# Kernel optimization log

Measured on AMD Instinct MI355X. Metric: run time of the kernel, lower is better.

## Reference

```python
import jax, jax.numpy as jnp
import numpy as np

D = 1024   # feature_dim
K = 10     # num_anchors
B = 16384  # batch
H = 8      # num_heads


def setup_inputs() -> dict:
    key = jax.random.key(0)
    ks = jax.random.split(key, 12)
    f32 = jnp.float32

    def w(k, shape, scale=0.02):
        return (jax.random.normal(k, shape, f32) * scale)

    return {
        "features": jax.random.normal(ks[0], (B, D), f32),
        "anchors": w(ks[1], (K, D), 0.1),
        # anchor_refiner: Linear(D, D//2) -> ReLU -> Linear(D//2, D) -> Tanh
        "ar_w1": w(ks[2], (D, D // 2)), "ar_b1": jnp.zeros((D // 2,), f32),
        "ar_w2": w(ks[3], (D // 2, D)), "ar_b2": jnp.zeros((D,), f32),
        # attention projections
        "q_w": w(ks[4], (D, D)), "q_b": jnp.zeros((D,), f32),
        "k_w": w(ks[5], (D, D)), "k_b": jnp.zeros((D,), f32),
        "v_w": w(ks[6], (D, D)), "v_b": jnp.zeros((D,), f32),
        "o_w": w(ks[7], (D, D)), "o_b": jnp.zeros((D,), f32),
        # feature_enhancer: LayerNorm -> Linear(D,2D) -> GELU -> Linear(2D,D)
        "ln_g": jnp.ones((D,), f32), "ln_b": jnp.zeros((D,), f32),
        "ff_w1": w(ks[8], (D, 2 * D)), "ff_b1": jnp.zeros((2 * D,), f32),
        "ff_w2": w(ks[9], (2 * D, D)), "ff_b2": jnp.zeros((D,), f32),
        "div_w": jnp.asarray(0.001, f32),
        "cen_w": jnp.asarray(0.001, f32),
    }


def _l2norm(x, eps=1e-8):
    n = jnp.linalg.norm(x, axis=-1, keepdims=True)
    return x / jnp.maximum(n, eps)


def _layernorm(x, g, b, eps=1e-5):
    mu = jnp.mean(x, axis=-1, keepdims=True)
    var = jnp.mean(jnp.square(x - mu), axis=-1, keepdims=True)
    return (x - mu) * jax.lax.rsqrt(var + eps) * g + b


def reference(features, anchors, ar_w1, ar_b1, ar_w2, ar_b2,
              q_w, q_b, k_w, k_b, v_w, v_b, o_w, o_b,
              ln_g, ln_b, ff_w1, ff_b1, ff_w2, ff_b2, div_w, cen_w):
    b = features.shape[0]
    hd = D // H
    fn = _l2norm(features)                                 # [B, D]

    # anchor refinement
    refin = jnp.tanh(jax.nn.relu(anchors @ ar_w1 + ar_b1) @ ar_w2 + ar_b2)
    an = _l2norm(anchors + 0.1 * refin)                    # [K, D]

    # multi-head cross-attention to anchors
    q = (fn @ q_w + q_b).reshape(b, H, hd)                 # [B, H, hd]
    k = (an @ k_w + k_b).reshape(K, H, hd)                 # [K, H, hd]
    v = (an @ v_w + v_b).reshape(K, H, hd)
    scores = jnp.einsum('bhd,khd->bhk', q, k) / jnp.sqrt(jnp.asarray(hd, fn.dtype))
    aw = jax.nn.softmax(scores, axis=-1)                   # [B, H, K]
    att = jnp.einsum('bhk,khd->bhd', aw, v).reshape(b, D)
    att = att @ o_w + o_b

    # feature enhancer (dropout inactive: eval mode)
    enh = fn + 0.1 * att
    h = jax.nn.gelu(_layernorm(enh, ln_g, ln_b) @ ff_w1 + ff_b1, approximate=False)
    enh = h @ ff_w2 + ff_b2
    final = fn + 0.2 * enh                                 # [B, D]

    # diversity loss: pdist over K=10 anchors (45 pairs)
    diff = an[:, None, :] - an[None, :, :]                 # [K, K, D]
    dmat = jnp.sqrt(jnp.maximum(jnp.sum(diff * diff, -1), 1e-24))
    iu = np.triu_indices(K, 1)
    div_loss = jnp.exp(-jnp.maximum(dmat[iu].mean(), 1e-6))

    # center loss: attention-weighted feature-anchor distances
    avg_att = aw.mean(axis=1)                              # [B, K]
    sq = (jnp.sum(fn * fn, 1, keepdims=True) + jnp.sum(an * an, 1)
          - 2.0 * fn @ an.T)
    fa_dist = jnp.sqrt(jnp.maximum(sq, 1e-12))             # [B, K]
    center_loss = jnp.sum(avg_att * fa_dist, axis=1).mean()

    geo = jnp.abs(div_w) * div_loss + jnp.abs(cen_w) * center_loss
    geo = jnp.clip(geo, 0.0, 0.01)
    return final, geo
```

## Files before the change

### kernel.cpp

```cpp
#include <hip/hip_runtime.h>
#include <hip/hip_bf16.h>
#include <math.h>

typedef __hip_bfloat16 bf16;

#define D_  1024
#define K_  10
#define B_  16384
#define H_  8
#define HD_ 128

struct alignas(16) BF8 { bf16 v[8]; };
struct alignas(8)  BF4 { bf16 v[4]; };

typedef __bf16 bf8v __attribute__((ext_vector_type(8)));
typedef float  f4v  __attribute__((ext_vector_type(4)));

__device__ __forceinline__ float b2f(bf16 x){ return __bfloat162float(x); }
__device__ __forceinline__ bf16  f2b(float x){ return __float2bfloat16(x); }

#define GL2LDS16(g, l) __builtin_amdgcn_global_load_lds( \
    (__attribute__((address_space(1))) void*)(g), \
    (__attribute__((address_space(3))) void*)(l), 16, 0, 0)

__global__ __launch_bounds__(256) void l2norm_k(const float* __restrict__ x,
                                                bf16* __restrict__ fnb) {
  int b = blockIdx.x, t = threadIdx.x;
  float4 v = ((const float4*)(x + (size_t)b * D_))[t];
  float p = v.x*v.x + v.y*v.y + v.z*v.z + v.w*v.w;
  #pragma unroll
  for (int o = 32; o > 0; o >>= 1) p += __shfl_down(p, o);
  __shared__ float wsum[4];
  if ((t & 63) == 0) wsum[t >> 6] = p;
  __syncthreads();
  __shared__ float inv_s;
  if (t == 0) inv_s = 1.f / fmaxf(sqrtf(wsum[0]+wsum[1]+wsum[2]+wsum[3]), 1e-8f);
  __syncthreads();
  float iv = inv_s;
  BF4 o;
  o.v[0] = f2b(v.x*iv); o.v[1] = f2b(v.y*iv);
  o.v[2] = f2b(v.z*iv); o.v[3] = f2b(v.w*iv);
  ((BF4*)(fnb + (size_t)b * D_))[t] = o;
}

__global__ __launch_bounds__(256) void wt_k(const float* __restrict__ w,
                                            bf16* __restrict__ wt, int R, int C) {
  __shared__ float tle[32][33];
  int c0 = blockIdx.x * 32, r0 = blockIdx.y * 32;
  int tx = threadIdx.x & 31, ty = threadIdx.x >> 5;
  #pragma unroll
  for (int i = 0; i < 32; i += 8)
    tle[ty + i][tx] = w[(size_t)(r0 + ty + i) * C + c0 + tx];
  __syncthreads();
  #pragma unroll
  for (int i = 0; i < 32; i += 8)
    wt[(size_t)(c0 + ty + i) * R + r0 + tx] = f2b(tle[tx][ty + i]);
}

template<int COLS, int KD, int ACT>
__global__ __launch_bounds__(256) void panelmm_k(
    const float* __restrict__ A, const float* __restrict__ W,
    const float* __restrict__ bias, const float* __restrict__ aux,
    float* __restrict__ out,
    const float* __restrict__ W2, const float* __restrict__ bias2,
    float* __restrict__ out2, int N, int npanel) {
  constexpr int GROUPS = 256 / COLS;
  constexpr int DCH = KD / GROUPS;
  __shared__ float A_s[K_][KD];
  __shared__ float part[K_][COLS][GROUPS];
  const int t = threadIdx.x;
  int blk = blockIdx.x;
  const float* Wm = W; const float* bm = bias; float* om = out;
  if (blk >= npanel) { blk -= npanel; Wm = W2; bm = bias2; om = out2; }
  const int panel = blk;
  for (int i = t; i < K_*KD; i += 256) A_s[0][i] = A[i];
  __syncthreads();
  const int cg = t % COLS, g = t / COLS;
  const int col = panel*COLS + cg;
  float s[K_];
  #pragma unroll
  for (int r = 0; r < K_; ++r) s[r] = 0.f;
  const float* wp = Wm + (size_t)(g*DCH)*N + col;
  for (int d = g*DCH; d < (g+1)*DCH; ++d) {
    float wv = *wp; wp += N;
    #pragma unroll
    for (int r = 0; r < K_; ++r) s[r] = fmaf(A_s[r][d], wv, s[r]);
  }
  #pragma unroll
  for (int r = 0; r < K_; ++r) part[r][cg][g] = s[r];
  __syncthreads();
  for (int o = t; o < K_*COLS; o += 256) {
    int r = o / COLS, c = o % COLS;
    float v = 0.f;
    #pragma unroll
    for (int gg = 0; gg < GROUPS; ++gg) v += part[r][c][gg];
    v += bm[panel*COLS + c];
    if constexpr (ACT == 1) v = fmaxf(v, 0.f);
    if constexpr (ACT == 2) v = aux[(size_t)r*N + panel*COLS + c] + 0.1f*tanhf(v);
    om[(size_t)r*N + panel*COLS + c] = v;
  }
}

template<int TRANSOUT, typename TW>
__global__ __launch_bounds__(256) void smallmm_k(
    const float* __restrict__ A, const TW* __restrict__ W,
    bf16* __restrict__ outb, float scale) {
  constexpr int COLS = 64, GROUPS = 4, DCH = 32, NW = 1024;
  __shared__ float A_s[K_][128];
  __shared__ float part[K_][COLS][GROUPS];
  const int t = threadIdx.x;
  const int h = blockIdx.x & 7, panel = blockIdx.x >> 3;
  for (int i = t; i < K_*128; i += 256) {
    int r = i >> 7, j = i & 127;
    A_s[r][j] = A[r*1024 + h*128 + j];
  }
  __syncthreads();
  const int cg = t % COLS, g = t / COLS;
  const int col = panel*COLS + cg;
  float s[K_];
  #pragma unroll
  for (int r = 0; r < K_; ++r) s[r] = 0.f;
  const TW* wp = W + (size_t)(h*128 + g*DCH)*NW + col;
  for (int d = g*DCH; d < g*DCH + DCH; ++d) {
    float wv;
    if constexpr (sizeof(TW) == 2) wv = b2f(*wp); else wv = *wp;
    wp += NW;
    #pragma unroll
    for (int r = 0; r < K_; ++r) s[r] = fmaf(A_s[r][d], wv, s[r]);
  }
  #pragma unroll
  for (int r = 0; r < K_; ++r) part[r][cg][g] = s[r];
  __syncthreads();
  for (int o = t; o < 16*COLS; o += 256) {
    int r = o / COLS, c = o % COLS;
    float v = 0.f;
    if (r < K_) {
      #pragma unroll
      for (int gg = 0; gg < GROUPS; ++gg) v += part[r][c][gg];
      v *= scale;
    }
    if constexpr (TRANSOUT) outb[(size_t)(panel*COLS + c)*128 + h*16 + r] = f2b(v);
    else                    outb[(size_t)(h*16 + r)*NW + panel*COLS + c] = f2b(v);
  }
}

__global__ void sbias_k(const float* __restrict__ qb, const float* __restrict__ Km,
                        float* __restrict__ sb) {
  int c = threadIdx.x;
  int h = c >> 4, k = c & 15;
  float s = 0.f;
  if (k < K_) {
    for (int j = 0; j < HD_; ++j)
      s = fmaf(qb[h*HD_ + j], Km[(size_t)k*D_ + h*HD_ + j], s);
  }
  sb[c] = s * 0.08838834764831845f;
}

__global__ __launch_bounds__(256) void ar3_k(const float* __restrict__ an_un,
    float* __restrict__ an, float* __restrict__ na, float* __restrict__ divloss) {
  __shared__ float a_s[K_][D_];
  __shared__ float nrm[K_];
  __shared__ float dm[45];
  const int t = threadIdx.x;
  for (int i = t; i < K_*D_; i += 256) a_s[0][i] = an_un[i];
  __syncthreads();
  const int wid = t >> 6, lane = t & 63;
  for (int r = wid; r < K_; r += 4) {
    float p = 0.f;
    for (int j = lane; j < D_; j += 64) p += a_s[r][j]*a_s[r][j];
    #pragma unroll
    for (int o = 1; o < 64; o <<= 1) p += __shfl_xor(p, o);
    if (lane == 0) nrm[r] = p;
  }
  __syncthreads();
  for (int i = t; i < K_*D_; i += 256) {
    int r = i >> 10;
    float iv = 1.f / fmaxf(sqrtf(nrm[r]), 1e-8f);
    float v = a_s[0][i] * iv;
    a_s[0][i] = v;
    an[i] = v;
  }
  if (t < K_) {
    float iv = 1.f / fmaxf(sqrtf(nrm[t]), 1e-8f);
    na[t] = nrm[t] * iv * iv;
  }
  __syncthreads();
  const int pr = t >> 2, sub = t & 3;
  if (pr < 45) {
    int i = 0, j = 0, c = pr;
    for (i = 0; i < K_; ++i) { int cnt = K_-1-i; if (c < cnt) { j = i+1+c; break; } c -= cnt; }
    float s = 0.f;
    for (int d = sub*256; d < sub*256 + 256; ++d) {
      float df = a_s[i][d] - a_s[j][d]; s += df*df;
    }
    s += __shfl_xor(s, 1); s += __shfl_xor(s, 2);
    if (sub == 0) dm[pr] = sqrtf(fmaxf(s, 1e-24f));
  }
  __syncthreads();
  if (t == 0) {
    float m = 0.f;
    for (int p = 0; p < 45; ++p) m += dm[p];
    m *= (1.f/45.f);
    *divloss = expf(-fmaxf(m, 1e-6f));
  }
}

template<int EPI, typename TO>
__global__ __launch_bounds__(256) void mgemm_k(
    const bf16* __restrict__ A, const bf16* __restrict__ Bt,
    const float* __restrict__ bias, const bf16* __restrict__ aux,
    TO* __restrict__ out, int M, int N, int Kd, float scale) {
  constexpr int BM = 128, BN = 128, BK = 32;
  __shared__ bf16 As[BM][BK];
  __shared__ bf16 Bs[BN][BK];
  const int tid = threadIdx.x;
  const int nMB = M / BM;
  const int nwg = gridDim.x;
  int wg = blockIdx.x;
  wg = (wg & 7) * (nwg >> 3) + (wg >> 3);
  const int mb = wg % nMB, nb = wg / nMB;
  const int bm = mb * BM, bn = nb * BN;

  const int srow = tid >> 2;
  const int sk   = (tid & 3) * 8;
  const bf16* ga = A  + (size_t)(bm + srow) * Kd + sk;
  const bf16* gb = Bt + (size_t)(bn + srow) * Kd + sk;
  const size_t rstep = (size_t)64 * Kd;
  bf16* la = &As[0][0] + tid * 8;
  bf16* lb = &Bs[0][0] + tid * 8;

  const int w    = tid >> 6;
  const int lane = tid & 63;
  const int wr = (w >> 1) * 64, wc = (w & 1) * 64;
  const int fr = lane & 15, fg = lane >> 4;

  f4v acc[4][4];
  const f4v zz = {0.f, 0.f, 0.f, 0.f};
  #pragma unroll
  for (int m = 0; m < 4; ++m)
    #pragma unroll
    for (int n = 0; n < 4; ++n) acc[m][n] = zz;

  for (int k0 = 0; k0 < Kd; k0 += BK) {
    GL2LDS16(ga,         la);
    GL2LDS16(ga + rstep, la + 2048);
    GL2LDS16(gb,         lb);
    GL2LDS16(gb + rstep, lb + 2048);
    __syncthreads();
    bf8v af[4], bf_[4];
    #pragma unroll
    for (int m = 0; m < 4; ++m)
      af[m] = *(const bf8v*)&As[wr + m*16 + fr][fg*8];
    #pragma unroll
    for (int n = 0; n < 4; ++n)
      bf_[n] = *(const bf8v*)&Bs[wc + n*16 + fr][fg*8];
    #pragma unroll
    for (int m = 0; m < 4; ++m)
      #pragma unroll
      for (int n = 0; n < 4; ++n)
        acc[m][n] = __builtin_amdgcn_mfma_f32_16x16x32_bf16(af[m], bf_[n], acc[m][n], 0, 0, 0);
    __syncthreads();
    ga += BK; gb += BK;
  }

  float bv[4];
  #pragma unroll
  for (int n = 0; n < 4; ++n) bv[n] = bias[bn + wc + n*16 + fr];
  #pragma unroll
  for (int m = 0; m < 4; ++m) {
    #pragma unroll
    for (int r = 0; r < 4; ++r) {
      const int row = bm + wr + m*16 + fg*4 + r;
      #pragma unroll
      for (int n = 0; n < 4; ++n) {
        const int col = bn + wc + n*16 + fr;
        float x = acc[m][n][r] + bv[n];
        if constexpr (EPI == 1) x = b2f(aux[(size_t)row * N + col]) + scale * x;
        if constexpr (EPI == 2) x = 0.5f * x * (1.f + erff(x * 0.70710678118654752f));
        if constexpr (sizeof(TO) == 2) out[(size_t)row * N + col] = f2b(x);
        else                           out[(size_t)row * N + col] = x;
      }
    }
  }
}

template<int EPI, typename TO>
__global__ __launch_bounds__(512, 2) void mgemm256_k(
    const bf16* __restrict__ A, const bf16* __restrict__ Bt,
    const float* __restrict__ bias, const bf16* __restrict__ aux,
    TO* __restrict__ out, int M, int N, int Kd, float scale) {
  constexpr int BM = 256, BN = 256, BK = 32, DEPTH = 3;
  __shared__ bf16 As[DEPTH][BM*BK];
  __shared__ bf16 Bs[DEPTH][BN*BK];
  const int tid = threadIdx.x;
  const int nMB = M / BM;
  const int nwg = gridDim.x;
  int wg = blockIdx.x;
  wg = (wg & 7) * (nwg >> 3) + (wg >> 3);
  const int bm = (wg % nMB) * BM, bn = (wg / nMB) * BN;

  const int sr = tid >> 2, ss = tid & 3;
  const int sx = ((ss ^ (sr & 3)) * 8);
  const bf16* gA0 = A  + (size_t)(bm + sr)       * Kd + sx;
  const bf16* gA1 = A  + (size_t)(bm + sr + 128) * Kd + sx;
  const bf16* gB0 = Bt + (size_t)(bn + sr)       * Kd + sx;
  const bf16* gB1 = Bt + (size_t)(bn + sr + 128) * Kd + sx;

  const int wid = tid >> 6, lane = tid & 63;
  const int wm = wid >> 2, wn = wid & 3;
  const int fr = lane & 15, fg = lane >> 4;
  const int slot = (fg ^ (fr & 3)) * 8;

  f4v acc[8][4];
  const f4v zz = {0.f, 0.f, 0.f, 0.f};
  #pragma unroll
  for (int m = 0; m < 8; ++m)
    #pragma unroll
    for (int n = 0; n < 4; ++n) acc[m][n] = zz;

  const int nt = Kd / BK;
  #pragma unroll
  for (int p = 0; p < DEPTH; ++p) {
    const int ko = p * BK;
    GL2LDS16(gA0 + ko, &As[p][0] + tid*8);
    GL2LDS16(gA1 + ko, &As[p][0] + tid*8 + 4096);
    GL2LDS16(gB0 + ko, &Bs[p][0] + tid*8);
    GL2LDS16(gB1 + ko, &Bs[p][0] + tid*8 + 4096);
  }

  int bufi = 0;
  for (int t = 0; t < nt; ++t) {
    const int rem = nt - 1 - t;
    if (rem >= 2)      asm volatile("s_waitcnt vmcnt(8)" ::: "memory");
    else if (rem == 1) asm volatile("s_waitcnt vmcnt(4)" ::: "memory");
    else               asm volatile("s_waitcnt vmcnt(0)" ::: "memory");
    __builtin_amdgcn_s_barrier();
    asm volatile("" ::: "memory");
    const bf16* la = &As[bufi][0];
    const bf16* lb = &Bs[bufi][0];
    bf8v af[8], bq[4];
    #pragma unroll
    for (int m = 0; m < 8; ++m)
      af[m] = *(const bf8v*)(la + (wm*128 + m*16 + fr)*BK + slot);
    #pragma unroll
    for (int n = 0; n < 4; ++n)
      bq[n] = *(const bf8v*)(lb + (wn*64 + n*16 + fr)*BK + slot);
    asm volatile("s_waitcnt lgkmcnt(0)" ::: "memory");
    __builtin_amdgcn_s_barrier();
    asm volatile("" ::: "memory");
    if (t + DEPTH < nt) {
      const int ko = (t + DEPTH) * BK;
      GL2LDS16(gA0 + ko, &As[bufi][0] + tid*8);
      GL2LDS16(gA1 + ko, &As[bufi][0] + tid*8 + 4096);
      GL2LDS16(gB0 + ko, &Bs[bufi][0] + tid*8);
      GL2LDS16(gB1 + ko, &Bs[bufi][0] + tid*8 + 4096);
    }
    __builtin_amdgcn_s_setprio(1);
    #pragma unroll
    for (int m = 0; m < 8; ++m)
      #pragma unroll
      for (int n = 0; n < 4; ++n)
        acc[m][n] = __builtin_amdgcn_mfma_f32_16x16x32_bf16(af[m], bq[n], acc[m][n], 0, 0, 0);
    __builtin_amdgcn_s_setprio(0);
    bufi = (bufi == DEPTH-1) ? 0 : bufi + 1;
  }

  float bv[4];
  #pragma unroll
  for (int n = 0; n < 4; ++n) bv[n] = bias[bn + wn*64 + n*16 + fr];
  #pragma unroll
  for (int m = 0; m < 8; ++m) {
    #pragma unroll
    for (int r = 0; r < 4; ++r) {
      const int row = bm + wm*128 + m*16 + fg*4 + r;
      #pragma unroll
      for (int n = 0; n < 4; ++n) {
        const int col = bn + wn*64 + n*16 + fr;
        float x = acc[m][n][r] + bv[n];
        if constexpr (EPI == 1) x = b2f(aux[(size_t)row * N + col]) + scale * x;
        if constexpr (EPI == 2) x = 0.5f * x * (1.f + erff(x * 0.70710678118654752f));
        if constexpr (sizeof(TO) == 2) out[(size_t)row * N + col] = f2b(x);
        else                           out[(size_t)row * N + col] = x;
      }
    }
  }
}

__device__ __forceinline__ BF8 pack8(float4 a, float4 b){
  BF8 o;
  o.v[0]=f2b(a.x); o.v[1]=f2b(a.y); o.v[2]=f2b(a.z); o.v[3]=f2b(a.w);
  o.v[4]=f2b(b.x); o.v[5]=f2b(b.y); o.v[6]=f2b(b.z); o.v[7]=f2b(b.w);
  return o;
}

__global__ __launch_bounds__(256) void attn2_k(
    const float* __restrict__ S, const bf16* __restrict__ fn,
    const float* __restrict__ an, const float* __restrict__ na,
    bf16* __restrict__ awp, float* __restrict__ cen_acc) {
  __shared__ bf16 Ab[K_][D_];
  __shared__ float na_s[K_];
  __shared__ float cred[4];
  const int t = threadIdx.x;
  for (int i = t*8; i < K_*D_; i += 2048) {
    float4 a0 = *(const float4*)(an+i), a1 = *(const float4*)(an+i+4);
    *(BF8*)(&Ab[0][0]+i) = pack8(a0, a1);
  }
  if (t < K_) na_s[t] = na[t];
  __syncthreads();
  const int wid = t >> 6, lane = t & 63;
  const int d0 = lane * 16;
  const int sub = lane & 7, head = lane >> 3;
  const int k0 = sub*2, k1 = k0 + 1;
  float na0 = (k0 < K_) ? na_s[k0] : 0.f;
  float na1 = (k1 < K_) ? na_s[k1] : 0.f;
  float c_acc = 0.f;
  const int row0 = blockIdx.x * 32 + wid * 8;

  for (int i = 0; i < 8; ++i) {
    const int row = row0 + i;
    float2 sv = *(const float2*)(S + (size_t)row*128 + head*16 + k0);
    float v0 = (k0 < K_) ? sv.x : -1e30f;
    float v1 = (k1 < K_) ? sv.y : -1e30f;
    float m = fmaxf(v0, v1);
    m = fmaxf(m, __shfl_xor(m,1)); m = fmaxf(m, __shfl_xor(m,2)); m = fmaxf(m, __shfl_xor(m,4));
    float e0 = (k0 < K_) ? __expf(v0 - m) : 0.f;
    float e1 = (k1 < K_) ? __expf(v1 - m) : 0.f;
    float es = e0 + e1;
    es += __shfl_xor(es,1); es += __shfl_xor(es,2); es += __shfl_xor(es,4);
    float inv = 1.f / es;
    float a0 = e0 * inv, a1 = e1 * inv;
    bf16 b0 = f2b(a0), b1 = f2b(a1);
    unsigned int pk = (unsigned int)(*(unsigned short*)&b0)
                    | ((unsigned int)(*(unsigned short*)&b1) << 16);
    *(unsigned int*)(awp + (size_t)row*128 + head*16 + k0) = pk;
    float g0 = a0, g1 = a1;
    g0 += __shfl_xor(g0,8); g0 += __shfl_xor(g0,16); g0 += __shfl_xor(g0,32);
    g1 += __shfl_xor(g1,8); g1 += __shfl_xor(g1,16); g1 += __shfl_xor(g1,32);
    const BF8* fr = (const BF8*)(fn + (size_t)row*D_) + lane*2;
    BF8 f0 = fr[0], f1 = fr[1];
    float fv[16];
    #pragma unroll
    for (int j = 0; j < 8; ++j) { fv[j] = b2f(f0.v[j]); fv[8+j] = b2f(f1.v[j]); }
    float my0 = 0.f, my1 = 0.f;
    #pragma unroll
    for (int k = 0; k < K_; ++k) {
      BF8 aa = *(const BF8*)&Ab[k][d0];
      BF8 ab = *(const BF8*)&Ab[k][d0 + 8];
      float s = 0.f;
      #pragma unroll
      for (int j = 0; j < 8; ++j) {
        s = fmaf(fv[j],   b2f(aa.v[j]), s);
        s = fmaf(fv[8+j], b2f(ab.v[j]), s);
      }
      #pragma unroll
      for (int o = 1; o < 64; o <<= 1) s += __shfl_xor(s, o);
      my0 = (k == k0) ? s : my0;
      my1 = (k == k1) ? s : my1;
    }
    if (sub < 5) {
      float dist0 = sqrtf(fmaxf(1.f + na0 - 2.f*my0, 1e-12f));
      float dist1 = sqrtf(fmaxf(1.f + na1 - 2.f*my1, 1e-12f));
      c_acc = fmaf(g0, dist0, c_acc);
      c_acc = fmaf(g1, dist1, c_acc);
    }
  }
  #pragma unroll
  for (int o = 1; o < 64; o <<= 1) c_acc += __shfl_xor(c_acc, o);
  if (lane == 0) cred[wid] = c_acc;
  __syncthreads();
  if (t == 0) {
    float s = (cred[0]+cred[1]+cred[2]+cred[3]) * (1.f/64.f/(float)B_);
    atomicAdd(cen_acc, s);
  }
}

__global__ __launch_bounds__(256) void ln_k(const bf16* __restrict__ x,
    const float* __restrict__ g, const float* __restrict__ bta,
    bf16* __restrict__ out) {
  int b = blockIdx.x, t = threadIdx.x;
  BF4 ld = ((const BF4*)(x + (size_t)b * D_))[t];
  float v[4];
  #pragma unroll
  for (int j = 0; j < 4; ++j) v[j] = b2f(ld.v[j]);
  float s = v[0]+v[1]+v[2]+v[3];
  #pragma unroll
  for (int o = 32; o > 0; o >>= 1) s += __shfl_down(s, o);
  __shared__ float w1[4], w2[4];
  if ((t & 63) == 0) w1[t >> 6] = s;
  __syncthreads();
  __shared__ float mu_s, rs_s;
  if (t == 0) mu_s = (w1[0]+w1[1]+w1[2]+w1[3]) * (1.f/D_);
  __syncthreads();
  float mu = mu_s;
  float qv = 0.f;
  #pragma unroll
  for (int j = 0; j < 4; ++j) { float d = v[j]-mu; qv += d*d; }
  #pragma unroll
  for (int o = 32; o > 0; o >>= 1) qv += __shfl_down(qv, o);
  if ((t & 63) == 0) w2[t >> 6] = qv;
  __syncthreads();
  if (t == 0) rs_s = rsqrtf((w2[0]+w2[1]+w2[2]+w2[3]) * (1.f/D_) + 1e-5f);
  __syncthreads();
  float rs = rs_s;
  BF4 o;
  #pragma unroll
  for (int j = 0; j < 4; ++j) {
    int col = t*4 + j;
    o.v[j] = f2b((v[j]-mu)*rs*g[col] + bta[col]);
  }
  ((BF4*)(out + (size_t)b * D_))[t] = o;
}

__global__ void geo_k(const float* __restrict__ divl, const float* __restrict__ cen,
                      const float* __restrict__ div_w, const float* __restrict__ cen_w,
                      float* __restrict__ out) {
  float g = fabsf(*div_w) * (*divl) + fabsf(*cen_w) * (*cen);
  out[0] = fminf(fmaxf(g, 0.f), 0.01f);
}

extern "C" void kernel_launch(void* const* d_in, const int* in_sizes, int n_in,
                              void* d_out, int out_size, void* d_ws, size_t ws_size,
                              hipStream_t stream) {
  const float* features = (const float*)d_in[0];
  const float* anchors  = (const float*)d_in[1];
  const float* ar_w1 = (const float*)d_in[2];
  const float* ar_b1 = (const float*)d_in[3];
  const float* ar_w2 = (const float*)d_in[4];
  const float* ar_b2 = (const float*)d_in[5];
  const float* q_w = (const float*)d_in[6];
  const float* q_b = (const float*)d_in[7];
  const float* k_w = (const float*)d_in[8];
  const float* k_b = (const float*)d_in[9];
  const float* v_w = (const float*)d_in[10];
  const float* v_b = (const float*)d_in[11];
  const float* o_w = (const float*)d_in[12];
  const float* o_b = (const float*)d_in[13];
  const float* ln_g = (const float*)d_in[14];
  const float* ln_b = (const float*)d_in[15];
  const float* ff_w1 = (const float*)d_in[16];
  const float* ff_b1 = (const float*)d_in[17];
  const float* ff_w2 = (const float*)d_in[18];
  const float* ff_b2 = (const float*)d_in[19];
  const float* div_w = (const float*)d_in[20];
  const float* cen_w = (const float*)d_in[21];
  float* out = (float*)d_out;

  char* w = (char*)d_ws;
  bf16* ws_fnb = (bf16*)w;  w += (size_t)B_ * D_ * 2;
  bf16* ws_enh = (bf16*)w;  w += (size_t)B_ * D_ * 2;
  bf16* ws_ln  = (bf16*)w;  w += (size_t)B_ * D_ * 2;
  bf16* ws_h   = (bf16*)w;  w += (size_t)B_ * 2048 * 2;
  float* ws_S  = (float*)w; w += (size_t)B_ * 128 * 4;
  bf16* ws_awp = (bf16*)w;  w += (size_t)B_ * 128 * 2;
  bf16* ws_wq  = (bf16*)w;  w += (size_t)D_ * D_ * 2;
  bf16* ws_w1t = (bf16*)w;  w += (size_t)D_ * 2048 * 2;
  bf16* ws_w2t = (bf16*)w;  w += (size_t)2048 * D_ * 2;
  bf16* ws_wt  = (bf16*)w;  w += (size_t)128 * D_ * 2;
  bf16* ws_vt  = (bf16*)w;  w += (size_t)D_ * 128 * 2;
  float* ws_har = (float*)w;  w += (size_t)K_ * (D_/2) * 4;
  float* ws_anu = (float*)w;  w += (size_t)K_ * D_ * 4;
  float* ws_an  = (float*)w;  w += (size_t)K_ * D_ * 4;
  float* ws_k   = (float*)w;  w += (size_t)K_ * D_ * 4;
  float* ws_v   = (float*)w;  w += (size_t)K_ * D_ * 4;
  float* ws_na  = (float*)w;  w += 256;
  float* ws_div = (float*)w;  w += 256;
  float* ws_cen = (float*)w;  w += 256;
  float* ws_sb  = (float*)w;  w += 512;
  if ((size_t)(w - (char*)d_ws) > ws_size) return;

  hipMemsetAsync(ws_cen, 0, 4, stream);

  wt_k<<<dim3(D_/32,   D_/32),   256, 0, stream>>>(q_w,   ws_wq,  D_,   D_);
  wt_k<<<dim3(2048/32, D_/32),   256, 0, stream>>>(ff_w1, ws_w1t, D_,   2048);
  wt_k<<<dim3(D_/32,   2048/32), 256, 0, stream>>>(ff_w2, ws_w2t, 2048, D_);

  l2norm_k<<<B_, 256, 0, stream>>>(features, ws_fnb);

  panelmm_k<32, 1024, 1><<<16, 256, 0, stream>>>(
      anchors, ar_w1, ar_b1, nullptr, ws_har,
      nullptr, nullptr, nullptr, D_/2, 16);
  panelmm_k<64, 512, 2><<<16, 256, 0, stream>>>(
      ws_har, ar_w2, ar_b2, anchors, ws_anu,
      nullptr, nullptr, nullptr, D_, 16);
  ar3_k<<<1, 256, 0, stream>>>(ws_anu, ws_an, ws_na, ws_div);
  panelmm_k<64, 1024, 0><<<32, 256, 0, stream>>>(
      ws_an, k_w, k_b, nullptr, ws_k,
      v_w, v_b, ws_v, D_, 16);

  smallmm_k<0, bf16><<<128, 256, 0, stream>>>(ws_k, ws_wq, ws_wt, 0.08838834764831845f);
  sbias_k<<<1, 128, 0, stream>>>(q_b, ws_k, ws_sb);
  smallmm_k<1, float><<<128, 256, 0, stream>>>(ws_v, o_w, ws_vt, 1.f);

  mgemm_k<0, float><<<dim3((B_/128)*(128/128)), 256, 0, stream>>>(
      ws_fnb, ws_wt, ws_sb, nullptr, ws_S, B_, 128, D_, 0.f);

  attn2_k<<<B_/32, 256, 0, stream>>>(ws_S, ws_fnb, ws_an, ws_na, ws_awp, ws_cen);

  mgemm256_k<1, bf16><<<dim3((B_/256)*(D_/256)), 512, 0, stream>>>(
      ws_awp, ws_vt, o_b, ws_fnb, ws_enh, B_, D_, 128, 0.1f);

  ln_k<<<B_, 256, 0, stream>>>(ws_enh, ln_g, ln_b, ws_ln);

  mgemm256_k<2, bf16><<<dim3((B_/256)*(2048/256)), 512, 0, stream>>>(
      ws_ln, ws_w1t, ff_b1, nullptr, ws_h, B_, 2048, D_, 0.f);

  mgemm256_k<1, float><<<dim3((B_/256)*(D_/256)), 512, 0, stream>>>(
      ws_h, ws_w2t, ff_b2, ws_fnb, out, B_, D_, 2048, 0.2f);

  geo_k<<<1, 1, 0, stream>>>(ws_div, ws_cen, div_w, cen_w, out + (size_t)B_ * D_);
}
```

Baseline: 446.1 us.

## Fold feature-anchor distances into score GEMM and deepen GEMM pipeline

Appends -2*anchor rows to the score weight matrix and 1+|a|^2 bias entries, so the score GEMM also produces squared feature-anchor distances, and the attention kernel stops re-reading the normalized features to compute dot products. The 256-tile GEMM also moves to a 4-stage LDS pipeline with prefetch issued right after the barrier, drops the second barrier per iteration, and splits the fragment loads to overlap with MFMAs. This doubles the score GEMM's N, raises LDS usage, and relies on a power-of-two DEPTH for the slot masking.

```diff
diff --git a/kernel.cpp b/kernel.cpp
--- a/kernel.cpp
+++ b/kernel.cpp
@@ -145,15 +145,36 @@
 }
 
 __global__ void sbias_k(const float* __restrict__ qb, const float* __restrict__ Km,
-                        float* __restrict__ sb) {
+                        const float* __restrict__ na, float* __restrict__ sb) {
   int c = threadIdx.x;
-  int h = c >> 4, k = c & 15;
-  float s = 0.f;
+  if (c < 128) {
+    int h = c >> 4, k = c & 15;
+    float s = 0.f;
+    if (k < K_) {
+      for (int j = 0; j < HD_; ++j)
+        s = fmaf(qb[h*HD_ + j], Km[(size_t)k*D_ + h*HD_ + j], s);
+    }
+    sb[c] = s * 0.08838834764831845f;
+  } else {
+    int j = c - 128;
+    sb[c] = (j < K_) ? (1.f + na[j]) : 0.f;
+  }
+}
+
+__global__ __launch_bounds__(256) void anext_k(const float* __restrict__ an,
+                                               bf16* __restrict__ wt) {
+  int k = blockIdx.x;
+  bf16* dst = wt + (size_t)(128 + k) * 1024;
+  int i = threadIdx.x * 4;
+  BF4 o;
   if (k < K_) {
-    for (int j = 0; j < HD_; ++j)
-      s = fmaf(qb[h*HD_ + j], Km[(size_t)k*D_ + h*HD_ + j], s);
-  }
-  sb[c] = s * 0.08838834764831845f;
+    float4 a = *(const float4*)(an + (size_t)k*1024 + i);
+    o.v[0] = f2b(-2.f*a.x); o.v[1] = f2b(-2.f*a.y);
+    o.v[2] = f2b(-2.f*a.z); o.v[3] = f2b(-2.f*a.w);
+  } else {
+    o.v[0] = o.v[1] = o.v[2] = o.v[3] = f2b(0.f);
+  }
+  *(BF4*)(dst + i) = o;
 }
 
 __global__ __launch_bounds__(256) void ar3_k(const float* __restrict__ an_un,
@@ -289,7 +310,7 @@
     const bf16* __restrict__ A, const bf16* __restrict__ Bt,
     const float* __restrict__ bias, const bf16* __restrict__ aux,
     TO* __restrict__ out, int M, int N, int Kd, float scale) {
-  constexpr int BM = 256, BN = 256, BK = 32, DEPTH = 3;
+  constexpr int BM = 256, BN = 256, BK = 32, DEPTH = 4;
   __shared__ bf16 As[DEPTH][BM*BK];
   __shared__ bf16 Bs[DEPTH][BN*BK];
   const int tid = threadIdx.x;
@@ -309,7 +330,7 @@
   const int wid = tid >> 6, lane = tid & 63;
   const int wm = wid >> 2, wn = wid & 3;
   const int fr = lane & 15, fg = lane >> 4;
-  const int slot = (fg ^ (fr & 3)) * 8;
+  const int rslot = (fg ^ (fr & 3)) * 8;
 
   f4v acc[8][4];
   const f4v zz = {0.f, 0.f, 0.f, 0.f};
@@ -320,49 +341,63 @@
 
   const int nt = Kd / BK;
   #pragma unroll
-  for (int p = 0; p < DEPTH; ++p) {
-    const int ko = p * BK;
-    GL2LDS16(gA0 + ko, &As[p][0] + tid*8);
-    GL2LDS16(gA1 + ko, &As[p][0] + tid*8 + 4096);
-    GL2LDS16(gB0 + ko, &Bs[p][0] + tid*8);
-    GL2LDS16(gB1 + ko, &Bs[p][0] + tid*8 + 4096);
-  }
-
-  int bufi = 0;
+  for (int p = 0; p < DEPTH-1; ++p) {
+    if (p < nt) {
+      const int ko = p * BK;
+      GL2LDS16(gA0 + ko, &As[p][0] + tid*8);
+      GL2LDS16(gA1 + ko, &As[p][0] + tid*8 + 4096);
+      GL2LDS16(gB0 + ko, &Bs[p][0] + tid*8);
+      GL2LDS16(gB1 + ko, &Bs[p][0] + tid*8 + 4096);
+    }
+  }
+
   for (int t = 0; t < nt; ++t) {
     const int rem = nt - 1 - t;
     if (rem >= 2)      asm volatile("s_waitcnt vmcnt(8)" ::: "memory");
     else if (rem == 1) asm volatile("s_waitcnt vmcnt(4)" ::: "memory");
     else               asm volatile("s_waitcnt vmcnt(0)" ::: "memory");
+    __builtin_amdgcn_sched_barrier(0);
     __builtin_amdgcn_s_barrier();
-    asm volatile("" ::: "memory");
-    const bf16* la = &As[bufi][0];
-    const bf16* lb = &Bs[bufi][0];
+    __builtin_amdgcn_sched_barrier(0);
+    if (t + DEPTH - 1 < nt) {
+      const int st = t + DEPTH - 1;
+      const int sl = st & (DEPTH-1);
+      const int ko = st * BK;
+      GL2LDS16(gA0 + ko, &As[sl][0] + tid*8);
+      GL2LDS16(gA1 + ko, &As[sl][0] + tid*8 + 4096);
+      GL2LDS16(gB0 + ko, &Bs[sl][0] + tid*8);
+      GL2LDS16(gB1 + ko, &Bs[sl][0] + tid*8 + 4096);
+    }
+    const int slot = t & (DEPTH-1);
+    const bf16* la = &As[slot][0];
+    const bf16* lb = &Bs[slot][0];
     bf8v af[8], bq[4];
     #pragma unroll
-    for (int m = 0; m < 8; ++m)
-      af[m] = *(const bf8v*)(la + (wm*128 + m*16 + fr)*BK + slot);
+    for (int m = 0; m < 4; ++m)
+      af[m] = *(const bf8v*)(la + (wm*128 + m*16 + fr)*BK + rslot);
     #pragma unroll
     for (int n = 0; n < 4; ++n)
-      bq[n] = *(const bf8v*)(lb + (wn*64 + n*16 + fr)*BK + slot);
+      bq[n] = *(const bf8v*)(lb + (wn*64 + n*16 + fr)*BK + rslot);
+    __builtin_amdgcn_sched_barrier(0);
+    #pragma unroll
+    for (int m = 4; m < 8; ++m)
+      af[m] = *(const bf8v*)(la + (wm*128 + m*16 + fr)*BK + rslot);
+    asm volatile("s_waitcnt lgkmcnt(4)" ::: "memory");
+    __builtin_amdgcn_sched_barrier(0);
+    __builtin_amdgcn_s_setprio(1);
+    #pragma unroll
+    for (int m = 0; m < 4; ++m)
+      #pragma unroll
+      for (int n = 0; n < 4; ++n)
+        acc[m][n] = __builtin_amdgcn_mfma_f32_16x16x32_bf16(af[m], bq[n], acc[m][n], 0, 0, 0);
     asm volatile("s_waitcnt lgkmcnt(0)" ::: "memory");
-    __builtin_amdgcn_s_barrier();
-    asm volatile("" ::: "memory");
-    if (t + DEPTH < nt) {
-      const int ko = (t + DEPTH) * BK;
-      GL2LDS16(gA0 + ko, &As[bufi][0] + tid*8);
-      GL2LDS16(gA1 + ko, &As[bufi][0] + tid*8 + 4096);
-      GL2LDS16(gB0 + ko, &Bs[bufi][0] + tid*8);
-      GL2LDS16(gB1 + ko, &Bs[bufi][0] + tid*8 + 4096);
-    }
-    __builtin_amdgcn_s_setprio(1);
-    #pragma unroll
-    for (int m = 0; m < 8; ++m)
+    __builtin_amdgcn_sched_barrier(0);
+    #pragma unroll
+    for (int m = 4; m < 8; ++m)
       #pragma unroll
       for (int n = 0; n < 4; ++n)
         acc[m][n] = __builtin_amdgcn_mfma_f32_16x16x32_bf16(af[m], bq[n], acc[m][n], 0, 0, 0);
     __builtin_amdgcn_s_setprio(0);
-    bufi = (bufi == DEPTH-1) ? 0 : bufi + 1;
   }
 
   float bv[4];
@@ -386,39 +421,21 @@
   }
 }
 
-__device__ __forceinline__ BF8 pack8(float4 a, float4 b){
-  BF8 o;
-  o.v[0]=f2b(a.x); o.v[1]=f2b(a.y); o.v[2]=f2b(a.z); o.v[3]=f2b(a.w);
-  o.v[4]=f2b(b.x); o.v[5]=f2b(b.y); o.v[6]=f2b(b.z); o.v[7]=f2b(b.w);
-  return o;
-}
-
 __global__ __launch_bounds__(256) void attn2_k(
-    const float* __restrict__ S, const bf16* __restrict__ fn,
-    const float* __restrict__ an, const float* __restrict__ na,
-    bf16* __restrict__ awp, float* __restrict__ cen_acc) {
-  __shared__ bf16 Ab[K_][D_];
-  __shared__ float na_s[K_];
+    const float* __restrict__ S, bf16* __restrict__ awp,
+    float* __restrict__ cen_acc) {
   __shared__ float cred[4];
   const int t = threadIdx.x;
-  for (int i = t*8; i < K_*D_; i += 2048) {
-    float4 a0 = *(const float4*)(an+i), a1 = *(const float4*)(an+i+4);
-    *(BF8*)(&Ab[0][0]+i) = pack8(a0, a1);
-  }
-  if (t < K_) na_s[t] = na[t];
-  __syncthreads();
   const int wid = t >> 6, lane = t & 63;
-  const int d0 = lane * 16;
   const int sub = lane & 7, head = lane >> 3;
   const int k0 = sub*2, k1 = k0 + 1;
-  float na0 = (k0 < K_) ? na_s[k0] : 0.f;
-  float na1 = (k1 < K_) ? na_s[k1] : 0.f;
   float c_acc = 0.f;
   const int row0 = blockIdx.x * 32 + wid * 8;
 
   for (int i = 0; i < 8; ++i) {
     const int row = row0 + i;
-    float2 sv = *(const float2*)(S + (size_t)row*128 + head*16 + k0);
+    const float* Sr = S + (size_t)row * 256;
+    float2 sv = *(const float2*)(Sr + head*16 + k0);
     float v0 = (k0 < K_) ? sv.x : -1e30f;
     float v1 = (k1 < K_) ? sv.y : -1e30f;
     float m = fmaxf(v0, v1);
@@ -436,32 +453,11 @@
     float g0 = a0, g1 = a1;
     g0 += __shfl_xor(g0,8); g0 += __shfl_xor(g0,16); g0 += __shfl_xor(g0,32);
     g1 += __shfl_xor(g1,8); g1 += __shfl_xor(g1,16); g1 += __shfl_xor(g1,32);
-    const BF8* fr = (const BF8*)(fn + (size_t)row*D_) + lane*2;
-    BF8 f0 = fr[0], f1 = fr[1];
-    float fv[16];
-    #pragma unroll
-    for (int j = 0; j < 8; ++j) { fv[j] = b2f(f0.v[j]); fv[8+j] = b2f(f1.v[j]); }
-    float my0 = 0.f, my1 = 0.f;
-    #pragma unroll
-    for (int k = 0; k < K_; ++k) {
-      BF8 aa = *(const BF8*)&Ab[k][d0];
-      BF8 ab = *(const BF8*)&Ab[k][d0 + 8];
-      float s = 0.f;
-      #pragma unroll
-      for (int j = 0; j < 8; ++j) {
-        s = fmaf(fv[j],   b2f(aa.v[j]), s);
-        s = fmaf(fv[8+j], b2f(ab.v[j]), s);
-      }
-      #pragma unroll
-      for (int o = 1; o < 64; o <<= 1) s += __shfl_xor(s, o);
-      my0 = (k == k0) ? s : my0;
-      my1 = (k == k1) ? s : my1;
-    }
     if (sub < 5) {
-      float dist0 = sqrtf(fmaxf(1.f + na0 - 2.f*my0, 1e-12f));
-      float dist1 = sqrtf(fmaxf(1.f + na1 - 2.f*my1, 1e-12f));
-      c_acc = fmaf(g0, dist0, c_acc);
-      c_acc = fmaf(g1, dist1, c_acc);
+      float d20 = Sr[128 + k0];
+      float d21 = Sr[128 + k1];
+      c_acc = fmaf(g0, sqrtf(fmaxf(d20, 1e-12f)), c_acc);
+      c_acc = fmaf(g1, sqrtf(fmaxf(d21, 1e-12f)), c_acc);
     }
   }
   #pragma unroll
@@ -550,12 +546,12 @@
   bf16* ws_enh = (bf16*)w;  w += (size_t)B_ * D_ * 2;
   bf16* ws_ln  = (bf16*)w;  w += (size_t)B_ * D_ * 2;
   bf16* ws_h   = (bf16*)w;  w += (size_t)B_ * 2048 * 2;
-  float* ws_S  = (float*)w; w += (size_t)B_ * 128 * 4;
+  float* ws_S  = (float*)w; w += (size_t)B_ * 256 * 4;
   bf16* ws_awp = (bf16*)w;  w += (size_t)B_ * 128 * 2;
   bf16* ws_wq  = (bf16*)w;  w += (size_t)D_ * D_ * 2;
   bf16* ws_w1t = (bf16*)w;  w += (size_t)D_ * 2048 * 2;
   bf16* ws_w2t = (bf16*)w;  w += (size_t)2048 * D_ * 2;
-  bf16* ws_wt  = (bf16*)w;  w += (size_t)128 * D_ * 2;
+  bf16* ws_wt  = (bf16*)w;  w += (size_t)256 * D_ * 2;
   bf16* ws_vt  = (bf16*)w;  w += (size_t)D_ * 128 * 2;
   float* ws_har = (float*)w;  w += (size_t)K_ * (D_/2) * 4;
   float* ws_anu = (float*)w;  w += (size_t)K_ * D_ * 4;
@@ -588,13 +584,14 @@
       v_w, v_b, ws_v, D_, 16);
 
   smallmm_k<0, bf16><<<128, 256, 0, stream>>>(ws_k, ws_wq, ws_wt, 0.08838834764831845f);
-  sbias_k<<<1, 128, 0, stream>>>(q_b, ws_k, ws_sb);
+  anext_k<<<128, 256, 0, stream>>>(ws_an, ws_wt);
+  sbias_k<<<1, 256, 0, stream>>>(q_b, ws_k, ws_na, ws_sb);
   smallmm_k<1, float><<<128, 256, 0, stream>>>(ws_v, o_w, ws_vt, 1.f);
 
-  mgemm_k<0, float><<<dim3((B_/128)*(128/128)), 256, 0, stream>>>(
-      ws_fnb, ws_wt, ws_sb, nullptr, ws_S, B_, 128, D_, 0.f);
-
-  attn2_k<<<B_/32, 256, 0, stream>>>(ws_S, ws_fnb, ws_an, ws_na, ws_awp, ws_cen);
+  mgemm_k<0, float><<<dim3((B_/128)*(256/128)), 256, 0, stream>>>(
+      ws_fnb, ws_wt, ws_sb, nullptr, ws_S, B_, 256, D_, 0.f);
+
+  attn2_k<<<B_/32, 256, 0, stream>>>(ws_S, ws_awp, ws_cen);
 
   mgemm256_k<1, bf16><<<dim3((B_/256)*(D_/256)), 512, 0, stream>>>(
       ws_awp, ws_vt, o_b, ws_fnb, ws_enh, B_, D_, 128, 0.1f);
```

Result: slower. 464.9 us (+4.2%).
